# Kernel optimization log

Measured on AMD Instinct MI355X. Metric: run time of the kernel, lower is better.

## Reference

```python
import jax, jax.numpy as jnp
import numpy as np
import math

B, H, W, K, E, FF, L, NH = 16, 64, 64, 2, 512, 2048, 4, 8


def setup_inputs() -> dict:
    key = jax.random.key(0)
    ks = jax.random.split(key, 24)
    s = 0.02
    inp = {
        "data": jax.random.normal(ks[0], (B, H, W), jnp.float32),
        "conv_w": jax.random.normal(ks[1], (K, K), jnp.float32) * 0.5,
        "conv_b": jax.random.normal(ks[2], (), jnp.float32) * 0.1,
        "lin_w": jax.random.normal(ks[3], (E, 1), jnp.float32) * 0.5,
        "lin_b": jax.random.normal(ks[4], (E,), jnp.float32) * 0.1,
        "Wq": jax.random.normal(ks[5], (L, E, E), jnp.float32) * s,
        "bq": jnp.zeros((L, E), jnp.float32),
        "Wk": jax.random.normal(ks[6], (L, E, E), jnp.float32) * s,
        "bk": jnp.zeros((L, E), jnp.float32),
        "Wv": jax.random.normal(ks[7], (L, E, E), jnp.float32) * s,
        "bv": jnp.zeros((L, E), jnp.float32),
        "Wo": jax.random.normal(ks[8], (L, E, E), jnp.float32) * s,
        "bo": jnp.zeros((L, E), jnp.float32),
        "ln1_g": jnp.ones((L, E), jnp.float32),
        "ln1_b": jnp.zeros((L, E), jnp.float32),
        "ln2_g": jnp.ones((L, E), jnp.float32),
        "ln2_b": jnp.zeros((L, E), jnp.float32),
        "W1": jax.random.normal(ks[9], (L, FF, E), jnp.float32) * s,
        "b1": jnp.zeros((L, FF), jnp.float32),
        "W2": jax.random.normal(ks[10], (L, E, FF), jnp.float32) * s,
        "b2": jnp.zeros((L, E), jnp.float32),
        "Wc": jax.random.normal(ks[11], (1, E), jnp.float32) * s,
        "bc": jnp.zeros((1,), jnp.float32),
        "num_heads": NH,
    }
    return inp


def _pos_encoding(seq_len, embed_dim):
    pos = jnp.arange(seq_len, dtype=jnp.float32)[:, None]
    div = jnp.exp(jnp.arange(0, embed_dim, 2, dtype=jnp.float32) * (-math.log(10000.0) / embed_dim))
    pe = jnp.zeros((seq_len, embed_dim), jnp.float32)
    pe = pe.at[:, 0::2].set(jnp.sin(pos * div))
    pe = pe.at[:, 1::2].set(jnp.cos(pos * div))
    return pe


def _layer_norm(x, g, b, eps=1e-5):
    mu = jnp.mean(x, axis=-1, keepdims=True)
    var = jnp.mean(jnp.square(x - mu), axis=-1, keepdims=True)
    return (x - mu) * jax.lax.rsqrt(var + eps) * g + b


def reference(data, conv_w, conv_b, lin_w, lin_b, Wq, bq, Wk, bk, Wv, bv, Wo, bo,
              ln1_g, ln1_b, ln2_g, ln2_b, W1, b1, W2, b2, Wc, bc, num_heads):
    b, h, w = data.shape
    k = conv_w.shape[0]
    # patch extraction == torch unfold(1,k,k).unfold(2,k,k) -> [B, P, k, k]
    patches = data.reshape(b, h // k, k, w // k, k).transpose(0, 1, 3, 2, 4)
    patches = patches.reshape(b, -1, k, k)
    # per-patch conv (k x k kernel on k x k patch -> scalar) + bias
    conv = jnp.einsum('bpij,ij->bp', patches, conv_w) + conv_b  # [B, P]
    # Linear(1 -> E)
    x = conv[..., None] * lin_w[:, 0] + lin_b  # [B, P, E]
    P, e = x.shape[1], x.shape[2]
    x = x + _pos_encoding(P, e)

    dk = e // num_heads
    scale = 1.0 / math.sqrt(dk)
    n_layers = Wq.shape[0]
    for l in range(n_layers):
        q = (x @ Wq[l].T + bq[l]).reshape(b, P, num_heads, dk).transpose(0, 2, 1, 3)
        kk = (x @ Wk[l].T + bk[l]).reshape(b, P, num_heads, dk).transpose(0, 2, 1, 3)
        v = (x @ Wv[l].T + bv[l]).reshape(b, P, num_heads, dk).transpose(0, 2, 1, 3)
        scores = jnp.einsum('bhqd,bhkd->bhqk', q, kk) * scale
        attn = jax.nn.softmax(scores, axis=-1)
        out = jnp.einsum('bhqk,bhkd->bhqd', attn, v)
        out = out.transpose(0, 2, 1, 3).reshape(b, P, e)
        out = out @ Wo[l].T + bo[l]
        x = _layer_norm(x + out, ln1_g[l], ln1_b[l])
        ffn = jax.nn.relu(x @ W1[l].T + b1[l]) @ W2[l].T + b2[l]
        x = _layer_norm(x + ffn, ln2_g[l], ln2_b[l])

    pooled = jnp.mean(x, axis=1)  # [B, E]
    return pooled @ Wc.T + bc  # [B, 1]
```

## Files before the change

### kernel.cpp

```cpp
#include <hip/hip_runtime.h>
#include <math.h>

#define P_SEQ 1024
#define E_DIM 512
#define NHEAD 8
#define DK    64
#define BATCH 16
#define M_TOK (BATCH * P_SEQ)
#define FF_DIM 2048
#define NLAYER 4

#define QSCALE 0.1803368801111204f

typedef __attribute__((ext_vector_type(8))) __bf16 bf16x8;
typedef __attribute__((ext_vector_type(4))) float floatx4;
typedef unsigned int u32;
typedef const __attribute__((address_space(1))) u32* gptr_t;
typedef __attribute__((address_space(3))) u32* lptr_t;

__device__ inline float bf2f(unsigned short u) {
  union { unsigned int i; float f; } c; c.i = ((unsigned int)u) << 16; return c.f;
}
__device__ inline unsigned short f2bf(float f) {
  union { float f; unsigned int i; } c; c.f = f;
  unsigned int i = c.i;
  i += 0x7FFFu + ((i >> 16) & 1u);
  return (unsigned short)(i >> 16);
}
__device__ inline bf16x8 ld8(const unsigned short* p) {
  return *reinterpret_cast<const bf16x8*>(p);
}

__device__ inline float fast_exp2(float x) {
#if defined(__HIP_DEVICE_COMPILE__) && __has_builtin(__builtin_amdgcn_exp2f)
  return __builtin_amdgcn_exp2f(x);
#else
  return exp2f(x);
#endif
}

__device__ inline unsigned int pkbf16(float lo, float hi) {
#if defined(__HIP_DEVICE_COMPILE__) && __has_builtin(__builtin_amdgcn_cvt_pk_bf16_f32)
  typedef __attribute__((ext_vector_type(2))) __bf16 bf16x2;
  bf16x2 v = __builtin_amdgcn_cvt_pk_bf16_f32(lo, hi);
  return __builtin_bit_cast(unsigned int, v);
#else
  return (unsigned int)f2bf(lo) | ((unsigned int)f2bf(hi) << 16);
#endif
}

__global__ void detect_dtype(const unsigned short* __restrict__ data, int* __restrict__ flag) {
  if (threadIdx.x == 0) {
    int sane = 0;
    for (int i = 0; i < 256; i++) {
      int e = (data[i] >> 7) & 0xFF;
      if (e >= 107 && e <= 133) sane++;
    }
    *flag = (sane >= 240) ? 0 : 1;
  }
}

#define C_DATA 0
#define C_WO   65536
#define C_BO   1114112
#define C_LN1G 1116160
#define C_LN1B 1118208
#define C_LN2G 1120256
#define C_LN2B 1122304
#define C_W1   1124352
#define C_B1   5318656
#define C_W2   5326848
#define C_B2   9521152
#define C_CW   9523200
#define C_CB   9523208
#define C_LW   9523216
#define C_LB   9523728
#define C_WC   9524240
#define C_BC   9524752

struct ConvArgs {
  const void* src[23];
  unsigned short* canon;
  unsigned short* wqkv;
  unsigned short* bqkv;
  const int* flag;
};

__global__ __launch_bounds__(256) void convert_pack(ConvArgs a)
{
  const int i = blockIdx.x * 256 + threadIdx.x;
  const bool f32 = (*a.flag != 0);
  #define LOADF(IDX, J) (f32 ? ((const float*)a.src[IDX])[J] \
                             : bf2f(((const unsigned short*)a.src[IDX])[J]))
  int base = 0;
  if (i < base + 1048576) {
    const int j = i - base, l = j >> 18, rem = j & 262143;
    a.wqkv[l * 786432 + rem] = f2bf(LOADF(5, j) * QSCALE);
    return;
  } base += 1048576;
  if (i < base + 1048576) {
    const int j = i - base, l = j >> 18, rem = j & 262143;
    a.wqkv[l * 786432 + 262144 + rem] = f2bf(LOADF(7, j));
    return;
  } base += 1048576;
  if (i < base + 1048576) {
    const int j = i - base, l = j >> 18, rem = j & 262143;
    a.wqkv[l * 786432 + 524288 + rem] = f2bf(LOADF(9, j));
    return;
  } base += 1048576;
  if (i < base + 4194304) {
    const int j = i - base;
    a.canon[C_W1 + j] = f2bf(LOADF(17, j));
    return;
  } base += 4194304;
  if (i < base + 4194304) {
    const int j = i - base;
    a.canon[C_W2 + j] = f2bf(LOADF(19, j));
    return;
  } base += 4194304;
  if (i < base + 1048576) {
    const int j = i - base;
    a.canon[C_WO + j] = f2bf(LOADF(11, j));
    return;
  } base += 1048576;
  if (i < base + 65536) {
    const int j = i - base;
    a.canon[C_DATA + j] = f2bf(LOADF(0, j));
    return;
  } base += 65536;
  if (i < base + 2048) {
    const int j = i - base, l = j >> 9, r = j & 511;
    a.bqkv[l * 1536 + r] = f2bf(LOADF(6, j) * QSCALE);
    return;
  } base += 2048;
  if (i < base + 2048) {
    const int j = i - base, l = j >> 9, r = j & 511;
    a.bqkv[l * 1536 + 512 + r] = f2bf(LOADF(8, j));
    return;
  } base += 2048;
  if (i < base + 2048) {
    const int j = i - base, l = j >> 9, r = j & 511;
    a.bqkv[l * 1536 + 1024 + r] = f2bf(LOADF(10, j));
    return;
  } base += 2048;
  if (i < base + 2048) { a.canon[C_BO   + i - base] = f2bf(LOADF(12, i - base)); return; } base += 2048;
  if (i < base + 2048) { a.canon[C_LN1G + i - base] = f2bf(LOADF(13, i - base)); return; } base += 2048;
  if (i < base + 2048) { a.canon[C_LN1B + i - base] = f2bf(LOADF(14, i - base)); return; } base += 2048;
  if (i < base + 2048) { a.canon[C_LN2G + i - base] = f2bf(LOADF(15, i - base)); return; } base += 2048;
  if (i < base + 2048) { a.canon[C_LN2B + i - base] = f2bf(LOADF(16, i - base)); return; } base += 2048;
  if (i < base + 8192) { a.canon[C_B1   + i - base] = f2bf(LOADF(18, i - base)); return; } base += 8192;
  if (i < base + 2048) { a.canon[C_B2   + i - base] = f2bf(LOADF(20, i - base)); return; } base += 2048;
  if (i < base + 4)   { a.canon[C_CW + i - base] = f2bf(LOADF(1, i - base)); return; } base += 4;
  if (i < base + 1)   { a.canon[C_CB + i - base] = f2bf(LOADF(2, i - base)); return; } base += 1;
  if (i < base + 512) { a.canon[C_LW + i - base] = f2bf(LOADF(3, i - base)); return; } base += 512;
  if (i < base + 512) { a.canon[C_LB + i - base] = f2bf(LOADF(4, i - base)); return; } base += 512;
  if (i < base + 512) { a.canon[C_WC + i - base] = f2bf(LOADF(21, i - base)); return; } base += 512;
  if (i < base + 1)   { a.canon[C_BC + i - base] = f2bf(LOADF(22, i - base)); return; }
  #undef LOADF
}
#define CONV_TOTAL (3*1048576 + 2*4194304 + 1048576 + 65536 + 3*2048 + 7*2048 + 8192 - 2048 + 4 + 1 + 512 + 512 + 512 + 1)

#define BM 128
#define BN 128
#define BK 64

template <int MODE>
__global__ __launch_bounds__(256) void gemm_tile(
    const unsigned short* __restrict__ X, const unsigned short* __restrict__ W,
    const unsigned short* __restrict__ bias, unsigned short* __restrict__ Y,
    int M, int N, int Kd)
{
  __shared__ __align__(16) unsigned short As[2][BM * BK];
  __shared__ __align__(16) unsigned short Bs[2][BN * BK];

  const int tid  = threadIdx.x;
  const int lane = tid & 63;
  const int wave = tid >> 6;
  const int wm = wave & 1, wn = wave >> 1;
  const int col = lane & 15, quad = lane >> 4;

  const int m0 = blockIdx.y * BM;
  const int n0 = blockIdx.x * BN;

  const int srow = tid >> 3;
  const int scb  = tid & 7;

  floatx4 acc[4][4] = {};

  auto stage = [&](int kt, int buf) {
    #pragma unroll
    for (int i = 0; i < 4; i++) {
      const int r  = i * 32 + srow;
      const int cb = scb ^ (r & 7);
      const unsigned short* ga = X + (size_t)(m0 + r) * Kd + kt + cb * 8;
      __builtin_amdgcn_global_load_lds((gptr_t)(const void*)ga,
          (lptr_t)(void*)&As[buf][r * BK + scb * 8], 16, 0, 0);
    }
    #pragma unroll
    for (int i = 0; i < 4; i++) {
      const int r  = i * 32 + srow;
      const int cb = scb ^ ((r >> 2) & 7);
      const unsigned short* gb = W + (size_t)(n0 + r) * Kd + kt + cb * 8;
      __builtin_amdgcn_global_load_lds((gptr_t)(const void*)gb,
          (lptr_t)(void*)&Bs[buf][r * BK + scb * 8], 16, 0, 0);
    }
  };

  const int NT = Kd / BK;
  stage(0, 0);

  for (int c = 0; c < NT; c++) {
    const int buf = c & 1;
    __syncthreads();
    if (c + 1 < NT) stage((c + 1) * BK, buf ^ 1);

    #pragma unroll
    for (int kk = 0; kk < 2; kk++) {
      bf16x8 af[4], bfr[4];
      #pragma unroll
      for (int t = 0; t < 4; t++) {
        const int mr = wm * 64 + t * 16 + col;
        const int ka = (kk * 4 + quad) ^ (mr & 7);
        af[t] = ld8(&As[buf][mr * BK + ka * 8]);
        const int nr = wn * 64 + col * 4 + t;
        const int kb = (kk * 4 + quad) ^ (col & 7);
        bfr[t] = ld8(&Bs[buf][nr * BK + kb * 8]);
      }
      #pragma unroll
      for (int mt = 0; mt < 4; mt++)
        #pragma unroll
        for (int nt = 0; nt < 4; nt++)
          acc[mt][nt] = __builtin_amdgcn_mfma_f32_16x16x32_bf16(af[mt], bfr[nt], acc[mt][nt], 0, 0, 0);
    }
  }

  const int col4 = n0 + wn * 64 + col * 4;
  float bb[4];
  {
    const uint2 bu = *reinterpret_cast<const uint2*>(&bias[col4]);
    bb[0] = bf2f((unsigned short)(bu.x & 0xffffu));
    bb[1] = bf2f((unsigned short)(bu.x >> 16));
    bb[2] = bf2f((unsigned short)(bu.y & 0xffffu));
    bb[3] = bf2f((unsigned short)(bu.y >> 16));
  }

  if (MODE == 4 && (col4 >> 9) == 2) {
    const int cc0 = col4 & 511;
    const int h = cc0 >> 6;
    #pragma unroll
    for (int nt = 0; nt < 4; nt++) {
      const int d = (cc0 + nt) & 63;
      #pragma unroll
      for (int mt = 0; mt < 4; mt++) {
        const int p0 = m0 + wm * 64 + mt * 16 + quad * 4;
        const int b = p0 >> 10, p = p0 & 1023;
        float v0 = acc[mt][nt][0] + bb[nt], v1 = acc[mt][nt][1] + bb[nt];
        float v2 = acc[mt][nt][2] + bb[nt], v3 = acc[mt][nt][3] + bb[nt];
        const size_t idx = 16777216 + (((size_t)(b * NHEAD + h) * DK) + d) * P_SEQ + p;
        *reinterpret_cast<uint2*>(&Y[idx]) = make_uint2(pkbf16(v0, v1), pkbf16(v2, v3));
      }
    }
  } else {
    const int third = col4 >> 9;
    const int cc0 = col4 & 511;
    const int h = cc0 >> 6, d0 = cc0 & 63;
    #pragma unroll
    for (int mt = 0; mt < 4; mt++) {
      #pragma unroll
      for (int r = 0; r < 4; r++) {
        const int rr = m0 + wm * 64 + mt * 16 + quad * 4 + r;
        float v0 = acc[mt][0][r] + bb[0], v1 = acc[mt][1][r] + bb[1];
        float v2 = acc[mt][2][r] + bb[2], v3 = acc[mt][3][r] + bb[3];
        if (MODE == 1) {
          v0 = fmaxf(v0, 0.f); v1 = fmaxf(v1, 0.f);
          v2 = fmaxf(v2, 0.f); v3 = fmaxf(v3, 0.f);
        }
        size_t idx;
        if (MODE == 4) {
          const int b = rr >> 10, p = rr & 1023;
          idx = (size_t)third * 8388608 + (((size_t)(b * NHEAD + h) * P_SEQ) + p) * DK + d0;
        } else {
          idx = (size_t)rr * N + col4;
        }
        *reinterpret_cast<uint2*>(&Y[idx]) = make_uint2(pkbf16(v0, v1), pkbf16(v2, v3));
      }
    }
  }
}

typedef __attribute__((ext_vector_type(8))) unsigned short ushortx8;

__global__ __launch_bounds__(256, 4) void attn_flash8(
    const unsigned short* __restrict__ Q, const unsigned short* __restrict__ K,
    const unsigned short* __restrict__ Vt, unsigned short* __restrict__ O)
{
  __shared__ __align__(16) unsigned short Ks[2][64 * 64];
  __shared__ __align__(16) unsigned short Vs[2][64 * 64];
  __shared__ __align__(16) unsigned short Ps[4][16 * 64];

  const int tid  = threadIdx.x;
  const int lane = tid & 63;
  const int wave = tid >> 6;
  const int col  = lane & 15, quad = lane >> 4;
  const int bh = blockIdx.x & 127;
  const int qb0 = (blockIdx.x >> 7) * 128 + wave * 32;

  const unsigned short* Qh = Q  + (size_t)bh * P_SEQ * DK;
  const unsigned short* Kh = K  + (size_t)bh * P_SEQ * DK;
  const unsigned short* Vh = Vt + (size_t)bh * DK * P_SEQ;

  bf16x8 aq[2][2];
  #pragma unroll
  for (int t = 0; t < 2; t++) {
    aq[t][0] = ld8(Qh + (size_t)(qb0 + t * 16 + col) * DK + quad * 8);
    aq[t][1] = ld8(Qh + (size_t)(qb0 + t * 16 + col) * DK + 32 + quad * 8);
  }

  const ushortx8 one_raw = {0x3F80, 0x3F80, 0x3F80, 0x3F80, 0x3F80, 0x3F80, 0x3F80, 0x3F80};
  const bf16x8 ones = __builtin_bit_cast(bf16x8, one_raw);

  floatx4 o[2][4] = {};
  floatx4 lacc[2] = {};

  const int srow = tid >> 3;
  const int scb  = tid & 7;

  auto stage = [&](int kk, int buf) {
    #pragma unroll
    for (int i = 0; i < 2; i++) {
      const int r  = i * 32 + srow;
      const int cb = scb ^ (r & 7);
      __builtin_amdgcn_global_load_lds(
          (gptr_t)(const void*)(Kh + (size_t)(kk + r) * DK + cb * 8),
          (lptr_t)(void*)&Ks[buf][r * 64 + scb * 8], 16, 0, 0);
      __builtin_amdgcn_global_load_lds(
          (gptr_t)(const void*)(Vh + (size_t)r * P_SEQ + kk + cb * 8),
          (lptr_t)(void*)&Vs[buf][r * 64 + scb * 8], 16, 0, 0);
    }
  };

  stage(0, 0);

  for (int c = 0; c < 16; c++) {
    const int buf = c & 1;
    __syncthreads();
    if (c < 15) stage((c + 1) * 64, buf ^ 1);

    bf16x8 kb0[4], kb1[4];
    #pragma unroll
    for (int nt = 0; nt < 4; nt++) {
      const int kr = nt * 16 + col;
      kb0[nt] = ld8(&Ks[buf][kr * 64 + ((quad       ^ (kr & 7)) << 3)]);
      kb1[nt] = ld8(&Ks[buf][kr * 64 + (((4 + quad) ^ (kr & 7)) << 3)]);
    }

    floatx4 s[2][4] = {};
    #pragma unroll
    for (int t = 0; t < 2; t++)
      #pragma unroll
      for (int nt = 0; nt < 4; nt++) {
        s[t][nt] = __builtin_amdgcn_mfma_f32_16x16x32_bf16(aq[t][0], kb0[nt], s[t][nt], 0, 0, 0);
        s[t][nt] = __builtin_amdgcn_mfma_f32_16x16x32_bf16(aq[t][1], kb1[nt], s[t][nt], 0, 0, 0);
      }

    bf16x8 pa[2][2];
    #pragma unroll
    for (int t = 0; t < 2; t++) {
      #pragma unroll
      for (int r = 0; r < 4; r++) {
        const int row = quad * 4 + r;
        unsigned short* pr = &Ps[wave][row * 64];
        #pragma unroll
        for (int nt = 0; nt < 4; nt++) {
          const float p = fast_exp2(fminf(s[t][nt][r], 126.f));
          union { float f; unsigned int u; } pu; pu.f = p;
          const int key = nt * 16 + col;
          pr[(((key >> 3) ^ (row & 7)) << 3) | (key & 7)] = (unsigned short)(pu.u >> 16);
        }
      }
      __asm__ volatile("s_waitcnt lgkmcnt(0)" ::: "memory");
      pa[t][0] = ld8(&Ps[wave][col * 64 + ((quad       ^ (col & 7)) << 3)]);
      pa[t][1] = ld8(&Ps[wave][col * 64 + (((4 + quad) ^ (col & 7)) << 3)]);
      lacc[t] = __builtin_amdgcn_mfma_f32_16x16x32_bf16(pa[t][0], ones, lacc[t], 0, 0, 0);
      lacc[t] = __builtin_amdgcn_mfma_f32_16x16x32_bf16(pa[t][1], ones, lacc[t], 0, 0, 0);
    }

    #pragma unroll
    for (int dt = 0; dt < 4; dt++) {
      const int dr = dt * 16 + col;
      const bf16x8 v0 = ld8(&Vs[buf][dr * 64 + ((quad       ^ (dr & 7)) << 3)]);
      const bf16x8 v1 = ld8(&Vs[buf][dr * 64 + (((4 + quad) ^ (dr & 7)) << 3)]);
      #pragma unroll
      for (int t = 0; t < 2; t++) {
        o[t][dt] = __builtin_amdgcn_mfma_f32_16x16x32_bf16(pa[t][0], v0, o[t][dt], 0, 0, 0);
        o[t][dt] = __builtin_amdgcn_mfma_f32_16x16x32_bf16(pa[t][1], v1, o[t][dt], 0, 0, 0);
      }
    }
  }

  const int b = bh >> 3, h = bh & 7;
  #pragma unroll
  for (int t = 0; t < 2; t++) {
    #pragma unroll
    for (int r = 0; r < 4; r++) {
      const float inv = 1.f / lacc[t][r];
      unsigned short* pr = &Ps[wave][(quad * 4 + r) * 64];
      #pragma unroll
      for (int dt = 0; dt < 4; dt++)
        pr[dt * 16 + col] = f2bf(o[t][dt][r] * inv);
    }
    __asm__ volatile("s_waitcnt lgkmcnt(0)" ::: "memory");
    #pragma unroll
    for (int r = 0; r < 4; r++) {
      const int p = qb0 + t * 16 + quad * 4 + r;
      const uint2 v = *reinterpret_cast<const uint2*>(&Ps[wave][(quad * 4 + r) * 64 + col * 4]);
      *reinterpret_cast<uint2*>(&O[((size_t)(b * P_SEQ + p)) * E_DIM + h * DK + col * 4]) = v;
    }
  }
}

__global__ __launch_bounds__(256) void add_ln4(
    unsigned short* __restrict__ X, const unsigned short* __restrict__ R,
    const unsigned short* __restrict__ g, const unsigned short* __restrict__ bta)
{
  const int row  = blockIdx.x * 4 + (threadIdx.x >> 6);
  const int lane = threadIdx.x & 63;
  const size_t base = (size_t)row * E_DIM + lane * 8;

  uint4 xu = *reinterpret_cast<const uint4*>(X + base);
  uint4 ru = *reinterpret_cast<const uint4*>(R + base);
  unsigned int xs[4] = {xu.x, xu.y, xu.z, xu.w};
  unsigned int rs[4] = {ru.x, ru.y, ru.z, ru.w};

  float v[8];
  float s = 0.f;
  #pragma unroll
  for (int i = 0; i < 4; i++) {
    v[2*i]   = bf2f((unsigned short)(xs[i] & 0xffffu)) + bf2f((unsigned short)(rs[i] & 0xffffu));
    v[2*i+1] = bf2f((unsigned short)(xs[i] >> 16))     + bf2f((unsigned short)(rs[i] >> 16));
    s += v[2*i] + v[2*i+1];
  }
  #pragma unroll
  for (int off = 1; off < 64; off <<= 1) s += __shfl_xor(s, off, 64);
  const float mu = s * (1.f / 512.f);

  float var = 0.f;
  #pragma unroll
  for (int i = 0; i < 8; i++) { float d = v[i] - mu; var += d * d; }
  #pragma unroll
  for (int off = 1; off < 64; off <<= 1) var += __shfl_xor(var, off, 64);
  const float rstd = rsqrtf(var * (1.f / 512.f) + 1e-5f);

  unsigned int ow[4];
  #pragma unroll
  for (int i = 0; i < 4; i++) {
    int e0 = lane * 8 + 2 * i;
    float y0 = (v[2*i]   - mu) * rstd * bf2f(g[e0])     + bf2f(bta[e0]);
    float y1 = (v[2*i+1] - mu) * rstd * bf2f(g[e0 + 1]) + bf2f(bta[e0 + 1]);
    ow[i] = pkbf16(y0, y1);
  }
  *reinterpret_cast<uint4*>(X + base) = make_uint4(ow[0], ow[1], ow[2], ow[3]);
}

__global__ __launch_bounds__(64) void embed_kernel(
    const unsigned short* __restrict__ canon, unsigned short* __restrict__ X)
{
  const unsigned short* data   = canon + C_DATA;
  const unsigned short* conv_w = canon + C_CW;
  const unsigned short* conv_b = canon + C_CB;
  const unsigned short* lin_w  = canon + C_LW;
  const unsigned short* lin_b  = canon + C_LB;
  const int bp = blockIdx.x;
  const int b = bp >> 10, p = bp & 1023;
  const int ph = p >> 5, pw = p & 31;
  const unsigned short* dr = data + ((size_t)b * 64 + ph * 2) * 64 + pw * 2;
  const float c = bf2f(dr[0])  * bf2f(conv_w[0]) + bf2f(dr[1])  * bf2f(conv_w[1])
                + bf2f(dr[64]) * bf2f(conv_w[2]) + bf2f(dr[65]) * bf2f(conv_w[3])
                + bf2f(conv_b[0]);
  const int lane = threadIdx.x;
  unsigned int ow[4];
  #pragma unroll
  for (int i = 0; i < 4; i++) {
    const int e0 = lane * 8 + 2 * i;
    const float fr = __expf(-(float)e0 * (9.210340371976184f / 512.f));
    const float ang = (float)p * fr;
    const float v0 = c * bf2f(lin_w[e0])     + bf2f(lin_b[e0])     + sinf(ang);
    const float v1 = c * bf2f(lin_w[e0 + 1]) + bf2f(lin_b[e0 + 1]) + cosf(ang);
    ow[i] = pkbf16(v0, v1);
  }
  *reinterpret_cast<uint4*>(X + (size_t)bp * E_DIM + lane * 8) =
      make_uint4(ow[0], ow[1], ow[2], ow[3]);
}

__global__ __launch_bounds__(256) void classify_partial(
    const unsigned short* __restrict__ X, const unsigned short* __restrict__ Wc,
    float* __restrict__ partial)
{
  const int b = blockIdx.x, sl = blockIdx.y;
  const int tid = threadIdx.x;
  const unsigned short* xb = X + (size_t)b * P_SEQ * E_DIM + (size_t)sl * 128 * E_DIM;
  float s0 = 0.f, s1 = 0.f;
  for (int p = 0; p < 128; p++) {
    s0 += bf2f(xb[(size_t)p * E_DIM + tid]);
    s1 += bf2f(xb[(size_t)p * E_DIM + tid + 256]);
  }
  float acc = s0 * bf2f(Wc[tid]) + s1 * bf2f(Wc[tid + 256]);
  #pragma unroll
  for (int off = 1; off < 64; off <<= 1) acc += __shfl_xor(acc, off, 64);
  __shared__ float red[4];
  if ((tid & 63) == 0) red[tid >> 6] = acc;
  __syncthreads();
  if (tid == 0) partial[b * 8 + sl] = red[0] + red[1] + red[2] + red[3];
}

__global__ __launch_bounds__(64) void classify_final(
    const float* __restrict__ partial, const unsigned short* __restrict__ bc,
    void* __restrict__ out, const int* __restrict__ flag)
{
  const int b = threadIdx.x;
  if (b >= BATCH) return;
  float s = 0.f;
  #pragma unroll
  for (int i = 0; i < 8; i++) s += partial[b * 8 + i];
  float r = s * (1.f / 1024.f) + bf2f(bc[0]);
  if (*flag) ((float*)out)[b] = r;
  else       ((unsigned short*)out)[b] = f2bf(r);
}

extern "C" void kernel_launch(void* const* d_in, const int* in_sizes, int n_in,
                              void* d_out, int out_size, void* d_ws, size_t ws_size,
                              hipStream_t stream)
{
  char* ws = (char*)d_ws;
  const size_t MB = (size_t)1 << 20;

  unsigned short* canon = (unsigned short*)ws;
  int* flag = (int*)(ws + 176 * MB);
  float* partial = (float*)(ws + 176 * MB + 256);
  unsigned short* wqkv = (unsigned short*)(ws + 177 * MB);
  unsigned short* bqkv = (unsigned short*)(ws + 184 * MB);

  unsigned short* x    = (unsigned short*)(ws + 32 * MB);
  unsigned short* qb   = (unsigned short*)(ws + 48 * MB);
  unsigned short* attn = (unsigned short*)(ws + 96 * MB);
  unsigned short* hbuf = (unsigned short*)(ws + 112 * MB);
  unsigned short* obuf = (unsigned short*)(ws + 144 * MB);
  unsigned short* fbuf = attn;

  const unsigned short* kb  = qb + 8388608;
  const unsigned short* vtb = qb + 16777216;

  detect_dtype<<<1, 64, 0, stream>>>((const unsigned short*)d_in[0], flag);

  ConvArgs ca;
  for (int i = 0; i < 23; i++) ca.src[i] = d_in[i];
  ca.canon = canon; ca.wqkv = wqkv; ca.bqkv = bqkv; ca.flag = flag;
  convert_pack<<<(CONV_TOTAL + 255) / 256, 256, 0, stream>>>(ca);

  embed_kernel<<<dim3(M_TOK), dim3(64), 0, stream>>>(canon, x);

  for (int l = 0; l < NLAYER; l++) {
    const unsigned short* Wqkv_l = wqkv + (size_t)l * 1536 * 512;
    const unsigned short* bqkv_l = bqkv + l * 1536;
    const unsigned short* Wo_l = canon + C_WO + (size_t)l * E_DIM * E_DIM;
    const unsigned short* W1_l = canon + C_W1 + (size_t)l * FF_DIM * E_DIM;
    const unsigned short* W2_l = canon + C_W2 + (size_t)l * E_DIM * FF_DIM;

    gemm_tile<4><<<dim3(1536 / BN, M_TOK / BM), dim3(256), 0, stream>>>(
        x, Wqkv_l, bqkv_l, qb, M_TOK, 1536, E_DIM);

    attn_flash8<<<dim3((P_SEQ / 128) * BATCH * NHEAD), dim3(256), 0, stream>>>(
        qb, kb, vtb, attn);

    gemm_tile<0><<<dim3(E_DIM / BN, M_TOK / BM), dim3(256), 0, stream>>>(
        attn, Wo_l, canon + C_BO + l * E_DIM, obuf, M_TOK, E_DIM, E_DIM);
    add_ln4<<<dim3(M_TOK / 4), dim3(256), 0, stream>>>(
        x, obuf, canon + C_LN1G + l * E_DIM, canon + C_LN1B + l * E_DIM);

    gemm_tile<1><<<dim3(FF_DIM / BN, M_TOK / BM), dim3(256), 0, stream>>>(
        x, W1_l, canon + C_B1 + l * FF_DIM, hbuf, M_TOK, FF_DIM, E_DIM);
    gemm_tile<0><<<dim3(E_DIM / BN, M_TOK / BM), dim3(256), 0, stream>>>(
        hbuf, W2_l, canon + C_B2 + l * E_DIM, fbuf, M_TOK, E_DIM, FF_DIM);
    add_ln4<<<dim3(M_TOK / 4), dim3(256), 0, stream>>>(
        x, fbuf, canon + C_LN2G + l * E_DIM, canon + C_LN2B + l * E_DIM);
  }

  classify_partial<<<dim3(BATCH, 8), dim3(256), 0, stream>>>(x, canon + C_WC, partial);
  classify_final<<<dim3(1), dim3(64), 0, stream>>>(partial, canon + C_BC, d_out, flag);
}
```

Before: 1.043 ms.

## Replace LDS double buffering with register-prefetched single-buffer GEMM pipeline

The GEMM tile kernel drops its double-buffered LDS staging, which used direct global-to-LDS loads. Instead it prefetches the next K tile into registers and writes it to a single LDS buffer between two barriers. This halves LDS use, and the launch bound is raised to request three blocks per CU for higher occupancy. In exchange it adds a second barrier per iteration and more register pressure from the prefetch registers. Global-load latency is now hidden only by the MFMA work of one tile.

```diff
diff --git a/kernel.cpp b/kernel.cpp
--- a/kernel.cpp
+++ b/kernel.cpp
@@ -47,6 +47,10 @@
 #else
   return (unsigned int)f2bf(lo) | ((unsigned int)f2bf(hi) << 16);
 #endif
+}
+
+__device__ inline void lds_barrier() {
+  __asm__ volatile("s_waitcnt lgkmcnt(0)\n\ts_barrier" ::: "memory");
 }
 
 __global__ void detect_dtype(const unsigned short* __restrict__ data, int* __restrict__ flag) {
@@ -165,13 +169,13 @@
 #define BK 64
 
 template <int MODE>
-__global__ __launch_bounds__(256) void gemm_tile(
+__global__ __launch_bounds__(256, 3) void gemm_tile(
     const unsigned short* __restrict__ X, const unsigned short* __restrict__ W,
     const unsigned short* __restrict__ bias, unsigned short* __restrict__ Y,
     int M, int N, int Kd)
 {
-  __shared__ __align__(16) unsigned short As[2][BM * BK];
-  __shared__ __align__(16) unsigned short Bs[2][BN * BK];
+  __shared__ __align__(16) unsigned short As[BM * BK];
+  __shared__ __align__(16) unsigned short Bs[BN * BK];
 
   const int tid  = threadIdx.x;
   const int lane = tid & 63;
@@ -187,33 +191,33 @@
 
   floatx4 acc[4][4] = {};
 
-  auto stage = [&](int kt, int buf) {
+  uint4 ar[4], br[4];
+  const unsigned short* xb = X + (size_t)(m0 + srow) * Kd + scb * 8;
+  const unsigned short* wb = W + (size_t)(n0 + srow) * Kd + scb * 8;
+
+  auto load_regs = [&](int kt) {
     #pragma unroll
     for (int i = 0; i < 4; i++) {
-      const int r  = i * 32 + srow;
-      const int cb = scb ^ (r & 7);
-      const unsigned short* ga = X + (size_t)(m0 + r) * Kd + kt + cb * 8;
-      __builtin_amdgcn_global_load_lds((gptr_t)(const void*)ga,
-          (lptr_t)(void*)&As[buf][r * BK + scb * 8], 16, 0, 0);
-    }
+      ar[i] = *reinterpret_cast<const uint4*>(xb + (size_t)(i * 32) * Kd + kt);
+      br[i] = *reinterpret_cast<const uint4*>(wb + (size_t)(i * 32) * Kd + kt);
+    }
+  };
+  auto write_lds = [&]() {
     #pragma unroll
     for (int i = 0; i < 4; i++) {
-      const int r  = i * 32 + srow;
-      const int cb = scb ^ ((r >> 2) & 7);
-      const unsigned short* gb = W + (size_t)(n0 + r) * Kd + kt + cb * 8;
-      __builtin_amdgcn_global_load_lds((gptr_t)(const void*)gb,
-          (lptr_t)(void*)&Bs[buf][r * BK + scb * 8], 16, 0, 0);
+      const int r = i * 32 + srow;
+      *reinterpret_cast<uint4*>(&As[r * BK + ((scb ^ (r & 7)) << 3)]) = ar[i];
+      *reinterpret_cast<uint4*>(&Bs[r * BK + ((scb ^ ((r >> 2) & 7)) << 3)]) = br[i];
     }
   };
 
   const int NT = Kd / BK;
-  stage(0, 0);
+  load_regs(0);
+  write_lds();
+  if (NT > 1) load_regs(BK);
+  lds_barrier();
 
   for (int c = 0; c < NT; c++) {
-    const int buf = c & 1;
-    __syncthreads();
-    if (c + 1 < NT) stage((c + 1) * BK, buf ^ 1);
-
     #pragma unroll
     for (int kk = 0; kk < 2; kk++) {
       bf16x8 af[4], bfr[4];
@@ -221,16 +225,22 @@
       for (int t = 0; t < 4; t++) {
         const int mr = wm * 64 + t * 16 + col;
         const int ka = (kk * 4 + quad) ^ (mr & 7);
-        af[t] = ld8(&As[buf][mr * BK + ka * 8]);
+        af[t] = ld8(&As[mr * BK + ka * 8]);
         const int nr = wn * 64 + col * 4 + t;
         const int kb = (kk * 4 + quad) ^ (col & 7);
-        bfr[t] = ld8(&Bs[buf][nr * BK + kb * 8]);
+        bfr[t] = ld8(&Bs[nr * BK + kb * 8]);
       }
       #pragma unroll
       for (int mt = 0; mt < 4; mt++)
         #pragma unroll
         for (int nt = 0; nt < 4; nt++)
           acc[mt][nt] = __builtin_amdgcn_mfma_f32_16x16x32_bf16(af[mt], bfr[nt], acc[mt][nt], 0, 0, 0);
+    }
+    if (c + 1 < NT) {
+      lds_barrier();
+      write_lds();
+      if (c + 2 < NT) load_regs((c + 2) * BK);
+      lds_barrier();
     }
   }
 
```

After: 2.533 ms. 2.43x slower.
